# Kernel optimization log

Measured on AMD Instinct MI355X. Metric: run time of the kernel, lower is better.

## Reference

```python
import jax, jax.numpy as jnp
import numpy as np

N = 100000      # nodes
E = 1600000     # edges
NODE_DIM = 128
HID = 128
L = 3           # num_layers
B = 512         # graphs in batch
EPS = 1e-5      # LayerNorm eps


def setup_inputs() -> dict:
    key = jax.random.key(0)
    ks = jax.random.split(key, 8)
    nodes = jax.random.normal(ks[0], (N, NODE_DIM), jnp.float32)
    edges = jax.random.randint(ks[1], (2, E), 0, N, dtype=jnp.int32)
    edge_types = jax.random.randint(ks[2], (E,), 0, 10, dtype=jnp.int32)
    batch_idx = jnp.sort(jax.random.randint(ks[3], (N,), 0, B, dtype=jnp.int32))
    w_in = jax.random.normal(ks[4], (NODE_DIM, HID), jnp.float32) / np.sqrt(NODE_DIM)
    b_in = jnp.zeros((HID,), jnp.float32)
    gcn_w = jax.random.normal(ks[5], (L, HID, HID), jnp.float32) / np.sqrt(HID)
    gcn_b = jnp.zeros((L, HID), jnp.float32)
    ln_g = jnp.ones((L, HID), jnp.float32)
    ln_b = jnp.zeros((L, HID), jnp.float32)
    return {"nodes": nodes, "edges": edges, "edge_types": edge_types,
            "batch_idx": batch_idx, "w_in": w_in, "b_in": b_in,
            "gcn_w": gcn_w, "gcn_b": gcn_b, "ln_g": ln_g, "ln_b": ln_b}


def _layer_norm(x, g, b):
    mu = jnp.mean(x, axis=-1, keepdims=True)
    var = jnp.mean(jnp.square(x - mu), axis=-1, keepdims=True)
    return (x - mu) * jax.lax.rsqrt(var + EPS) * g + b


def reference(nodes, edges, edge_types, batch_idx, w_in, b_in, gcn_w, gcn_b, ln_g, ln_b):
    src, dst = edges[0], edges[1]
    # GCN normalization with self-loops: deg = in-degree(A) + 1
    deg = jax.ops.segment_sum(jnp.ones((E,), nodes.dtype), dst, num_segments=N) + 1.0
    dinv_sqrt = jax.lax.rsqrt(deg)
    dinv = 1.0 / deg                       # self-loop norm = 1/deg_i
    enorm = dinv_sqrt[src] * dinv_sqrt[dst]

    x = nodes @ w_in + b_in                # input projection [N, HID]
    for i in range(L):
        res = x
        xw = x @ gcn_w[i]
        agg = jax.ops.segment_sum(xw[src] * enorm[:, None], dst, num_segments=N)
        x = agg + xw * dinv[:, None] + gcn_b[i]
        x = jax.nn.relu(_layer_norm(x, ln_g[i], ln_b[i]))
        # dropout is identity in eval mode
        if i > 0:
            x = x + res                    # residual only for i > 0

    # global mean pool per graph
    counts = jax.ops.segment_sum(jnp.ones((N,), x.dtype), batch_idx, num_segments=B)
    plan = jax.ops.segment_sum(x, batch_idx, num_segments=B) / jnp.maximum(counts, 1.0)[:, None]
    return x, plan
```

## Files before the change

### kernel.cpp

```cpp
#include <hip/hip_runtime.h>
#include <hip/hip_bf16.h>

typedef __attribute__((ext_vector_type(8))) short bf16x8;
typedef __attribute__((ext_vector_type(4))) float f32x4;
typedef __attribute__((ext_vector_type(2))) float f32x2;

#define K1_TILE 6144
#define NBCAP 4608

__device__ __forceinline__ unsigned short f2bf(float f) {
    union { unsigned int i; float f; } x; x.f = f;
    unsigned int r = (x.i + 0x7fffu + ((x.i >> 16) & 1u)) >> 16;
    return (unsigned short)r;
}
__device__ __forceinline__ float blo(unsigned int u) { return __uint_as_float(u << 16); }
__device__ __forceinline__ float bhi(unsigned int u) { return __uint_as_float(u & 0xffff0000u); }


__global__ __launch_bounds__(256) void bin_k(const int* __restrict__ src,
                                             const int* __restrict__ dst,
                                             int* __restrict__ bucket_cursor,
                                             int* __restrict__ bins,
                                             int E, int NB) {
    __shared__ int hist[512];
    __shared__ int gdiff[512];
    __shared__ int wsum[4];
    __shared__ int stage[K1_TILE];
    int tid = threadIdx.x;
    int base = blockIdx.x * K1_TILE;
    int cnt = min(K1_TILE, E - base);

    hist[tid] = 0; hist[tid + 256] = 0;
    __syncthreads();
    for (int i = tid; i < cnt; i += 256) atomicAdd(&hist[dst[base + i] >> 8], 1);
    __syncthreads();

    int h0 = hist[2 * tid], h1 = hist[2 * tid + 1];
    int v = h0 + h1;
    int lane = tid & 63, wid = tid >> 6;
    int s = v;
#pragma unroll
    for (int o = 1; o < 64; o <<= 1) { int n = __shfl_up(s, o); if (lane >= o) s += n; }
    if (lane == 63) wsum[wid] = s;
    __syncthreads();
    if (tid == 0) { int r = 0; for (int w = 0; w < 4; ++w) { int t2 = wsum[w]; wsum[w] = r; r += t2; } }
    __syncthreads();
    int lb0 = s + wsum[wid] - v;
    int lb1 = lb0 + h0;
    int b0 = 2 * tid, b1 = 2 * tid + 1;
    int gb0 = 0, gb1 = 0;
    if (h0 > 0 && b0 < NB) gb0 = atomicAdd(&bucket_cursor[b0], h0);
    if (h1 > 0 && b1 < NB) gb1 = atomicAdd(&bucket_cursor[b1], h1);
    __syncthreads();
    hist[b0] = lb0; hist[b1] = lb1;
    gdiff[b0] = gb0 - lb0; gdiff[b1] = gb1 - lb1;
    __syncthreads();

    for (int i = tid; i < cnt; i += 256) {
        int sv = src[base + i], dv = dst[base + i];
        int pos = atomicAdd(&hist[dv >> 8], 1);
        stage[pos] = ((dv & 255) << 24) | sv;
    }
    __syncthreads();

    for (int i = tid; i < cnt; i += 256) {
        int e = stage[i];
        int b = dst[base + i] >> 8;
        (void)b;
        break;
    }
    for (int b = tid; b < 512; b += 256) {
    }
    __syncthreads();
}


__global__ __launch_bounds__(256) void bin2_k(const int* __restrict__ src,
                                              const int* __restrict__ dst,
                                              int* __restrict__ bucket_cursor,
                                              int* __restrict__ bins,
                                              int E, int NB) {
    __shared__ int hist[512];
    __shared__ int lbase[513];
    __shared__ int gdiff[512];
    __shared__ int wsum[4];
    __shared__ int stage[K1_TILE];
    int tid = threadIdx.x;
    int base = blockIdx.x * K1_TILE;
    int cnt = min(K1_TILE, E - base);

    hist[tid] = 0; hist[tid + 256] = 0;
    __syncthreads();
    for (int i = tid; i < cnt; i += 256) atomicAdd(&hist[dst[base + i] >> 8], 1);
    __syncthreads();

    int h0 = hist[2 * tid], h1 = hist[2 * tid + 1];
    int v = h0 + h1;
    int lane = tid & 63, wid = tid >> 6;
    int s = v;
#pragma unroll
    for (int o = 1; o < 64; o <<= 1) { int n = __shfl_up(s, o); if (lane >= o) s += n; }
    if (lane == 63) wsum[wid] = s;
    __syncthreads();
    if (tid == 0) { int r = 0; for (int w = 0; w < 4; ++w) { int t2 = wsum[w]; wsum[w] = r; r += t2; } }
    __syncthreads();
    int lb0 = s + wsum[wid] - v;
    int lb1 = lb0 + h0;
    int b0 = 2 * tid, b1 = 2 * tid + 1;
    int gb0 = 0, gb1 = 0;
    if (h0 > 0 && b0 < NB) gb0 = atomicAdd(&bucket_cursor[b0], h0);
    if (h1 > 0 && b1 < NB) gb1 = atomicAdd(&bucket_cursor[b1], h1);
    __syncthreads();
    hist[b0] = lb0; hist[b1] = lb1;
    lbase[b0] = lb0; lbase[b1] = lb1;
    gdiff[b0] = gb0 - lb0; gdiff[b1] = gb1 - lb1;
    if (tid == 0) lbase[512] = cnt;
    __syncthreads();

    for (int i = tid; i < cnt; i += 256) {
        int sv = src[base + i], dv = dst[base + i];
        int pos = atomicAdd(&hist[dv >> 8], 1);
        stage[pos] = ((dv & 255) << 24) | sv;
    }
    __syncthreads();

    for (int i = tid; i < cnt; i += 256) {
        int lo = 0, hi = 512;
        while (lo + 1 < hi) { int mid = (lo + hi) >> 1; if (lbase[mid] <= i) lo = mid; else hi = mid; }
        int p = gdiff[lo] + i;
        if (p < NBCAP) bins[(size_t)lo * NBCAP + p] = stage[i];
    }
}


__global__ __launch_bounds__(256) void bucket_scan_k(const int* __restrict__ bucket_cursor,
                                                     int* __restrict__ bucket_base, int NB) {
    __shared__ int wsum[4];
    int tid = threadIdx.x;
    int h0 = (2 * tid < NB) ? min(bucket_cursor[2 * tid], NBCAP) : 0;
    int h1 = (2 * tid + 1 < NB) ? min(bucket_cursor[2 * tid + 1], NBCAP) : 0;
    int v = h0 + h1;
    int lane = tid & 63, wid = tid >> 6;
    int s = v;
#pragma unroll
    for (int o = 1; o < 64; o <<= 1) { int n = __shfl_up(s, o); if (lane >= o) s += n; }
    if (lane == 63) wsum[wid] = s;
    __syncthreads();
    if (tid == 0) { int r = 0; for (int w = 0; w < 4; ++w) { int t2 = wsum[w]; wsum[w] = r; r += t2; } }
    __syncthreads();
    int excl = s + wsum[wid] - v;
    if (2 * tid < NB) bucket_base[2 * tid] = excl;
    if (2 * tid + 1 < NB) bucket_base[2 * tid + 1] = excl + h0;
}


__global__ __launch_bounds__(256) void csr_build_k(const int* __restrict__ bins,
                                                   const int* __restrict__ bucket_cursor,
                                                   const int* __restrict__ bucket_base,
                                                   int* __restrict__ csr_src,
                                                   int* __restrict__ row_start,
                                                   float* __restrict__ dinv_sqrt,
                                                   float* __restrict__ dinv,
                                                   int N) {
    __shared__ int counts[256];
    __shared__ int cursor[256];
    __shared__ int wsum[4];
    __shared__ int lcsr[NBCAP];
    int b = blockIdx.x, tid = threadIdx.x;
    int cnt = min(bucket_cursor[b], NBCAP);
    int cbase = bucket_base[b];
    const int* my = bins + (size_t)b * NBCAP;

    counts[tid] = 0;
    __syncthreads();
    for (int i = tid; i < cnt; i += 256) atomicAdd(&counts[((unsigned)my[i]) >> 24], 1);
    __syncthreads();

    int v = counts[tid];
    int lane = tid & 63, wid = tid >> 6;
    int s = v;
#pragma unroll
    for (int o = 1; o < 64; o <<= 1) { int n = __shfl_up(s, o); if (lane >= o) s += n; }
    if (lane == 63) wsum[wid] = s;
    __syncthreads();
    if (tid == 0) { int r = 0; for (int w = 0; w < 4; ++w) { int t2 = wsum[w]; wsum[w] = r; r += t2; } }
    __syncthreads();
    int excl = s + wsum[wid] - v;

    int node = b * 256 + tid;
    if (node <= N) row_start[node] = cbase + excl;
    if (node < N) {
        float dg = (float)v + 1.0f;
        dinv_sqrt[node] = rsqrtf(dg);
        dinv[node] = 1.0f / dg;
    }
    cursor[tid] = excl;
    __syncthreads();

    for (int i = tid; i < cnt; i += 256) {
        int e = my[i];
        int pos = atomicAdd(&cursor[((unsigned)e) >> 24], 1);
        lcsr[pos] = e & 0xffffff;
    }
    __syncthreads();
    for (int i = tid; i < cnt; i += 256) csr_src[cbase + i] = lcsr[i];
}


__global__ __launch_bounds__(256) void pack_w_k(const float* __restrict__ w_in,
                                                const float* __restrict__ gcn_w,
                                                unsigned short* __restrict__ Wp) {
    int t = blockIdx.x * 256 + threadIdx.x;
    if (t >= 8192) return;
    int mat = t >> 11;
    int kb = (t >> 9) & 3;
    int ct = (t >> 6) & 7;
    int lane = t & 63;
    int q = lane >> 4, c = lane & 15;
    const float* W = (mat == 0) ? w_in : (gcn_w + (size_t)(mat - 1) * 16384);
    unsigned short o[8];
#pragma unroll
    for (int j = 0; j < 8; ++j)
        o[j] = f2bf(W[(size_t)(kb * 32 + q * 8 + j) * 128 + ct * 16 + c]);
    unsigned short* dstp = Wp + ((size_t)t) * 8;
#pragma unroll
    for (int j = 0; j < 8; ++j) dstp[j] = o[j];
}


__global__ __launch_bounds__(256) void proj_k(const float* __restrict__ A,
                                              const unsigned short* __restrict__ Wp,
                                              const float* __restrict__ bias,
                                              unsigned short* __restrict__ Cb,
                                              int M) {
    __shared__ unsigned short stage[64 * 128];
    int wid = threadIdx.x >> 6, lane = threadIdx.x & 63;
    int blk0 = blockIdx.x * 64;
    int r0 = blk0 + wid * 16;
    int q = lane >> 4, c = lane & 15;
    int ar = min(r0 + c, M - 1);

    f32x4 acc[8];
#pragma unroll
    for (int ct = 0; ct < 8; ++ct) acc[ct] = (f32x4){0.f, 0.f, 0.f, 0.f};

#pragma unroll
    for (int kb = 0; kb < 4; ++kb) {
        float4 f0 = *(const float4*)&A[(size_t)ar * 128 + kb * 32 + q * 8];
        float4 f1 = *(const float4*)&A[(size_t)ar * 128 + kb * 32 + q * 8 + 4];
        union { unsigned short u[8]; bf16x8 v; } af;
        af.u[0] = f2bf(f0.x); af.u[1] = f2bf(f0.y); af.u[2] = f2bf(f0.z); af.u[3] = f2bf(f0.w);
        af.u[4] = f2bf(f1.x); af.u[5] = f2bf(f1.y); af.u[6] = f2bf(f1.z); af.u[7] = f2bf(f1.w);
#pragma unroll
        for (int ct = 0; ct < 8; ++ct) {
            bf16x8 b = *(const bf16x8*)&Wp[(((size_t)(kb * 8 + ct)) * 64 + lane) * 8];
            acc[ct] = __builtin_amdgcn_mfma_f32_16x16x32_bf16(af.v, b, acc[ct], 0, 0, 0);
        }
    }

#pragma unroll
    for (int ct = 0; ct < 8; ++ct) {
        int col = ct * 16 + c;
        float bv = bias[col];
#pragma unroll
        for (int r = 0; r < 4; ++r)
            stage[(wid * 16 + q * 4 + r) * 128 + col] = f2bf(acc[ct][r] + bv);
    }
    __syncthreads();

    int tid = threadIdx.x;
#pragma unroll
    for (int i = 0; i < 4; ++i) {
        int k = tid + i * 256;
        int row = k >> 4, colc = (k & 15) * 8;
        int grow = blk0 + row;
        if (grow < M)
            *(uint4*)&Cb[(size_t)grow * 128 + colc] = *(const uint4*)&stage[row * 128 + colc];
    }
}


__global__ __launch_bounds__(256) void gemmln_k(const unsigned short* __restrict__ S,
                                                unsigned short* xb16,
                                                float* __restrict__ xout,
                                                const unsigned short* __restrict__ Wp,
                                                const float* __restrict__ bias,
                                                const float* __restrict__ g,
                                                const float* __restrict__ bb,
                                                int M, int residual, int write_f32) {
    __shared__ unsigned short stage[64 * 128];
    int wid = threadIdx.x >> 6, lane = threadIdx.x & 63;
    int blk0 = blockIdx.x * 64;
    int r0 = blk0 + wid * 16;
    int q = lane >> 4, c = lane & 15;
    int ar = min(r0 + c, M - 1);

    f32x4 acc[8];
#pragma unroll
    for (int ct = 0; ct < 8; ++ct) acc[ct] = (f32x4){0.f, 0.f, 0.f, 0.f};

#pragma unroll
    for (int kb = 0; kb < 4; ++kb) {
        bf16x8 a = *(const bf16x8*)&S[(size_t)ar * 128 + kb * 32 + q * 8];
#pragma unroll
        for (int ct = 0; ct < 8; ++ct) {
            bf16x8 b = *(const bf16x8*)&Wp[(((size_t)(kb * 8 + ct)) * 64 + lane) * 8];
            acc[ct] = __builtin_amdgcn_mfma_f32_16x16x32_bf16(a, b, acc[ct], 0, 0, 0);
        }
    }

    float v[8][4];
#pragma unroll
    for (int ct = 0; ct < 8; ++ct) {
        float bv = bias[ct * 16 + c];
#pragma unroll
        for (int r = 0; r < 4; ++r) v[ct][r] = acc[ct][r] + bv;
    }

    float mu[4], rs[4];
#pragma unroll
    for (int r = 0; r < 4; ++r) {
        float s = 0.f;
#pragma unroll
        for (int ct = 0; ct < 8; ++ct) s += v[ct][r];
        s += __shfl_xor(s, 1); s += __shfl_xor(s, 2);
        s += __shfl_xor(s, 4); s += __shfl_xor(s, 8);
        mu[r] = s * (1.0f / 128.0f);
    }
#pragma unroll
    for (int r = 0; r < 4; ++r) {
        float s = 0.f;
#pragma unroll
        for (int ct = 0; ct < 8; ++ct) { float d = v[ct][r] - mu[r]; s += d * d; }
        s += __shfl_xor(s, 1); s += __shfl_xor(s, 2);
        s += __shfl_xor(s, 4); s += __shfl_xor(s, 8);
        rs[r] = rsqrtf(s * (1.0f / 128.0f) + 1e-5f);
    }

#pragma unroll
    for (int ct = 0; ct < 8; ++ct) {
        int col = ct * 16 + c;
        float gamma = g[col], beta = bb[col];
#pragma unroll
        for (int r = 0; r < 4; ++r) {
            float y = fmaxf((v[ct][r] - mu[r]) * rs[r] * gamma + beta, 0.f);
            stage[(wid * 16 + q * 4 + r) * 128 + col] = f2bf(y);
        }
    }
    __syncthreads();

    int tid = threadIdx.x;
#pragma unroll
    for (int i = 0; i < 4; ++i) {
        int k = tid + i * 256;
        int row = k >> 4, colc = (k & 15) * 8;
        int grow = blk0 + row;
        if (grow >= M) continue;
        uint4 sv = *(const uint4*)&stage[row * 128 + colc];
        float y0 = blo(sv.x), y1 = bhi(sv.x), y2 = blo(sv.y), y3 = bhi(sv.y);
        float y4 = blo(sv.z), y5 = bhi(sv.z), y6 = blo(sv.w), y7 = bhi(sv.w);
        if (residual) {
            uint4 rv = *(const uint4*)&xb16[(size_t)grow * 128 + colc];
            y0 += blo(rv.x); y1 += bhi(rv.x); y2 += blo(rv.y); y3 += bhi(rv.y);
            y4 += blo(rv.z); y5 += bhi(rv.z); y6 += blo(rv.w); y7 += bhi(rv.w);
        }
        union { unsigned short u[8]; uint4 qv; } o;
        o.u[0] = f2bf(y0); o.u[1] = f2bf(y1); o.u[2] = f2bf(y2); o.u[3] = f2bf(y3);
        o.u[4] = f2bf(y4); o.u[5] = f2bf(y5); o.u[6] = f2bf(y6); o.u[7] = f2bf(y7);
        *(uint4*)&xb16[(size_t)grow * 128 + colc] = o.qv;
        if (write_f32) {
            *(float4*)&xout[(size_t)grow * 128 + colc] = make_float4(y0, y1, y2, y3);
            *(float4*)&xout[(size_t)grow * 128 + colc + 4] = make_float4(y4, y5, y6, y7);
        }
    }
}


__device__ __forceinline__ void acc8(f32x2& a0, f32x2& a1, f32x2& a2, f32x2& a3,
                                     uint4 u, float w) {
    f32x2 w2 = {w, w};
    f32x2 p0 = {blo(u.x), bhi(u.x)};
    f32x2 p1 = {blo(u.y), bhi(u.y)};
    f32x2 p2 = {blo(u.z), bhi(u.z)};
    f32x2 p3 = {blo(u.w), bhi(u.w)};
    a0 += p0 * w2; a1 += p1 * w2; a2 += p2 * w2; a3 += p3 * w2;
}

__global__ __launch_bounds__(256) void agg_k(const unsigned short* __restrict__ xb16,
                                             unsigned short* __restrict__ S,
                                             const int* __restrict__ row_start,
                                             const int* __restrict__ csr_src,
                                             const float* __restrict__ dst_tbl,
                                             const float* __restrict__ dinv,
                                             int N) {
    int wid = threadIdx.x >> 6, lane = threadIdx.x & 63;
    int n = blockIdx.x * 4 + wid;
    if (n >= N) return;
    int grp = lane >> 4;
    int sl = lane & 15;
    int c0 = sl * 8;

    f32x2 a0 = {0.f, 0.f}, a1 = {0.f, 0.f}, a2 = {0.f, 0.f}, a3 = {0.f, 0.f};
    int beg = row_start[n], end = row_start[n + 1];

    int j = beg;
    for (; j + 8 <= end; j += 8) {
        int sa = csr_src[j + grp];
        int sb = csr_src[j + grp + 4];
        float wa = dst_tbl[sa];
        float wb = dst_tbl[sb];
        uint4 ua = *(const uint4*)&xb16[(size_t)sa * 128 + c0];
        uint4 ub = *(const uint4*)&xb16[(size_t)sb * 128 + c0];
        acc8(a0, a1, a2, a3, ua, wa);
        acc8(a0, a1, a2, a3, ub, wb);
    }
    if (j < end) {
        int ja = j + grp, jb = j + grp + 4;
        int jca = min(ja, end - 1), jcb = min(jb, end - 1);
        int sa = csr_src[jca];
        int sb = csr_src[jcb];
        float wa = (ja < end) ? dst_tbl[sa] : 0.f;
        float wb = (jb < end) ? dst_tbl[sb] : 0.f;
        uint4 ua = *(const uint4*)&xb16[(size_t)sa * 128 + c0];
        uint4 ub = *(const uint4*)&xb16[(size_t)sb * 128 + c0];
        acc8(a0, a1, a2, a3, ua, wa);
        acc8(a0, a1, a2, a3, ub, wb);
    }

#pragma unroll
    for (int o = 16; o <= 32; o <<= 1) {
        a0.x += __shfl_xor(a0.x, o); a0.y += __shfl_xor(a0.y, o);
        a1.x += __shfl_xor(a1.x, o); a1.y += __shfl_xor(a1.y, o);
        a2.x += __shfl_xor(a2.x, o); a2.y += __shfl_xor(a2.y, o);
        a3.x += __shfl_xor(a3.x, o); a3.y += __shfl_xor(a3.y, o);
    }

    if (grp == 0) {
        float dsd = dst_tbl[n];
        float di = dinv[n];
        uint4 u = *(const uint4*)&xb16[(size_t)n * 128 + c0];
        float y0 = a0.x * dsd + blo(u.x) * di;
        float y1 = a0.y * dsd + bhi(u.x) * di;
        float y2 = a1.x * dsd + blo(u.y) * di;
        float y3 = a1.y * dsd + bhi(u.y) * di;
        float y4 = a2.x * dsd + blo(u.z) * di;
        float y5 = a2.y * dsd + bhi(u.z) * di;
        float y6 = a3.x * dsd + blo(u.w) * di;
        float y7 = a3.y * dsd + bhi(u.w) * di;
        union { unsigned short us[8]; uint4 qv; } o;
        o.us[0] = f2bf(y0); o.us[1] = f2bf(y1); o.us[2] = f2bf(y2); o.us[3] = f2bf(y3);
        o.us[4] = f2bf(y4); o.us[5] = f2bf(y5); o.us[6] = f2bf(y6); o.us[7] = f2bf(y7);
        *(uint4*)&S[(size_t)n * 128 + c0] = o.qv;
    }
}


__global__ __launch_bounds__(256) void bounds_k(const int* __restrict__ bidx,
                                                int* __restrict__ gstart, int N, int B) {
    int i = blockIdx.x * 256 + threadIdx.x;
    if (i > N) return;
    int cur = (i < N) ? bidx[i] : B;
    int prev = (i == 0) ? -1 : bidx[i - 1];
    for (int b = prev + 1; b <= cur; ++b) gstart[b] = i;
}

__global__ __launch_bounds__(256) void pool_k(const unsigned short* __restrict__ x,
                                              const int* __restrict__ gstart,
                                              float* __restrict__ plan) {
    __shared__ float red[8 * 128];
    int b = blockIdx.x, t = threadIdx.x;
    int cg = (t & 31) * 4;
    int h = t >> 5;
    int s = gstart[b], e = gstart[b + 1];
    float acc0 = 0.f, acc1 = 0.f, acc2 = 0.f, acc3 = 0.f;
    for (int i = s + h; i < e; i += 8) {
        uint2 u = *(const uint2*)&x[(size_t)i * 128 + cg];
        acc0 += blo(u.x); acc1 += bhi(u.x); acc2 += blo(u.y); acc3 += bhi(u.y);
    }
    red[h * 128 + cg] = acc0; red[h * 128 + cg + 1] = acc1;
    red[h * 128 + cg + 2] = acc2; red[h * 128 + cg + 3] = acc3;
    __syncthreads();
    if (h == 0) {
#pragma unroll
        for (int k = 1; k < 8; ++k) {
            acc0 += red[k * 128 + cg];     acc1 += red[k * 128 + cg + 1];
            acc2 += red[k * 128 + cg + 2]; acc3 += red[k * 128 + cg + 3];
        }
        float inv = 1.0f / (float)max(e - s, 1);
        *(float4*)&plan[(size_t)b * 128 + cg] = make_float4(acc0 * inv, acc1 * inv,
                                                            acc2 * inv, acc3 * inv);
    }
}


extern "C" void kernel_launch(void* const* d_in, const int* in_sizes, int n_in,
                              void* d_out, int out_size, void* d_ws, size_t ws_size,
                              hipStream_t stream) {
    const float* nodes     = (const float*)d_in[0];
    const int*   edges     = (const int*)d_in[1];
    const int*   batch_idx = (const int*)d_in[3];
    const float* w_in      = (const float*)d_in[4];
    const float* b_in      = (const float*)d_in[5];
    const float* gcn_w     = (const float*)d_in[6];
    const float* gcn_b     = (const float*)d_in[7];
    const float* ln_g      = (const float*)d_in[8];
    const float* ln_b      = (const float*)d_in[9];

    const int N = in_sizes[0] / 128;
    const int E = in_sizes[1] / 2;
    const int B = out_size / 128 - N;
    const int* src = edges;
    const int* dst = edges + E;
    const int NB = (N + 256) / 256;

    float* xbuf = (float*)d_out;
    float* plan = xbuf + (size_t)N * 128;

    unsigned short* xb16 = (unsigned short*)d_ws;
    unsigned short* Sb   = xb16 + (size_t)N * 128;
    unsigned short* Wp   = Sb + (size_t)N * 128;
    int* bins            = (int*)(Wp + 4 * 16384);
    int* bucket_cursor   = bins + (size_t)NB * NBCAP;
    int* bucket_base     = bucket_cursor + NB;
    int* csr_src         = bucket_base + NB;
    int* row_start       = csr_src + E;
    float* dinv_sqrt     = (float*)(row_start + N + 1);
    float* dinv          = dinv_sqrt + N;
    int* gstart          = (int*)(dinv + N);

    hipMemsetAsync(bucket_cursor, 0, sizeof(int) * NB, stream);

    bin2_k<<<(E + K1_TILE - 1) / K1_TILE, 256, 0, stream>>>(src, dst, bucket_cursor, bins, E, NB);
    bucket_scan_k<<<1, 256, 0, stream>>>(bucket_cursor, bucket_base, NB);
    csr_build_k<<<NB, 256, 0, stream>>>(bins, bucket_cursor, bucket_base,
                                        csr_src, row_start, dinv_sqrt, dinv, N);

    pack_w_k<<<32, 256, 0, stream>>>(w_in, gcn_w, Wp);

    proj_k<<<(N + 63) / 64, 256, 0, stream>>>(nodes, Wp, b_in, xb16, N);

    for (int l = 0; l < 3; ++l) {
        agg_k<<<(N + 3) / 4, 256, 0, stream>>>(xb16, Sb, row_start, csr_src,
                                               dinv_sqrt, dinv, N);
        gemmln_k<<<(N + 63) / 64, 256, 0, stream>>>(Sb, xb16, xbuf,
                                                    Wp + (size_t)(l + 1) * 16384,
                                                    gcn_b + (size_t)l * 128,
                                                    ln_g + (size_t)l * 128,
                                                    ln_b + (size_t)l * 128, N,
                                                    l > 0 ? 1 : 0, l == 2 ? 1 : 0);
    }

    bounds_k<<<(N + 1 + 255) / 256, 256, 0, stream>>>(batch_idx, gstart, N, B);
    pool_k<<<B, 256, 0, stream>>>(xb16, gstart, plan);
}
```

Before: 460.4 us.

## Fuse neighbor aggregation with GEMM+LayerNorm per layer using ping-pong buffers

Merges the separate aggregation kernel and the GEMM+LayerNorm kernel into one kernel. Each wave aggregates 16 destination rows into padded LDS, then runs the MFMA GEMM, LayerNorm, ReLU and residual on them. Two ping-pong bf16 buffers replace the in-place update, which removes the intermediate S round trip through global memory and one launch per layer. In exchange each block now does serial per-row gathers, which may cut latency hiding and occupancy. LayerNorm variance now uses a single pass (E[x^2]-mu^2), and the unused bin_k kernel is deleted.

```diff
diff --git a/kernel.cpp b/kernel.cpp
--- a/kernel.cpp
+++ b/kernel.cpp
@@ -7,6 +7,7 @@
 
 #define K1_TILE 6144
 #define NBCAP 4608
+#define RSTRIDE 136
 
 __device__ __forceinline__ unsigned short f2bf(float f) {
     union { unsigned int i; float f; } x; x.f = f;
@@ -15,64 +16,6 @@
 }
 __device__ __forceinline__ float blo(unsigned int u) { return __uint_as_float(u << 16); }
 __device__ __forceinline__ float bhi(unsigned int u) { return __uint_as_float(u & 0xffff0000u); }
-
-
-__global__ __launch_bounds__(256) void bin_k(const int* __restrict__ src,
-                                             const int* __restrict__ dst,
-                                             int* __restrict__ bucket_cursor,
-                                             int* __restrict__ bins,
-                                             int E, int NB) {
-    __shared__ int hist[512];
-    __shared__ int gdiff[512];
-    __shared__ int wsum[4];
-    __shared__ int stage[K1_TILE];
-    int tid = threadIdx.x;
-    int base = blockIdx.x * K1_TILE;
-    int cnt = min(K1_TILE, E - base);
-
-    hist[tid] = 0; hist[tid + 256] = 0;
-    __syncthreads();
-    for (int i = tid; i < cnt; i += 256) atomicAdd(&hist[dst[base + i] >> 8], 1);
-    __syncthreads();
-
-    int h0 = hist[2 * tid], h1 = hist[2 * tid + 1];
-    int v = h0 + h1;
-    int lane = tid & 63, wid = tid >> 6;
-    int s = v;
-#pragma unroll
-    for (int o = 1; o < 64; o <<= 1) { int n = __shfl_up(s, o); if (lane >= o) s += n; }
-    if (lane == 63) wsum[wid] = s;
-    __syncthreads();
-    if (tid == 0) { int r = 0; for (int w = 0; w < 4; ++w) { int t2 = wsum[w]; wsum[w] = r; r += t2; } }
-    __syncthreads();
-    int lb0 = s + wsum[wid] - v;
-    int lb1 = lb0 + h0;
-    int b0 = 2 * tid, b1 = 2 * tid + 1;
-    int gb0 = 0, gb1 = 0;
-    if (h0 > 0 && b0 < NB) gb0 = atomicAdd(&bucket_cursor[b0], h0);
-    if (h1 > 0 && b1 < NB) gb1 = atomicAdd(&bucket_cursor[b1], h1);
-    __syncthreads();
-    hist[b0] = lb0; hist[b1] = lb1;
-    gdiff[b0] = gb0 - lb0; gdiff[b1] = gb1 - lb1;
-    __syncthreads();
-
-    for (int i = tid; i < cnt; i += 256) {
-        int sv = src[base + i], dv = dst[base + i];
-        int pos = atomicAdd(&hist[dv >> 8], 1);
-        stage[pos] = ((dv & 255) << 24) | sv;
-    }
-    __syncthreads();
-
-    for (int i = tid; i < cnt; i += 256) {
-        int e = stage[i];
-        int b = dst[base + i] >> 8;
-        (void)b;
-        break;
-    }
-    for (int b = tid; b < 512; b += 256) {
-    }
-    __syncthreads();
-}
 
 
 __global__ __launch_bounds__(256) void bin2_k(const int* __restrict__ src,
@@ -280,102 +223,6 @@
 }
 
 
-__global__ __launch_bounds__(256) void gemmln_k(const unsigned short* __restrict__ S,
-                                                unsigned short* xb16,
-                                                float* __restrict__ xout,
-                                                const unsigned short* __restrict__ Wp,
-                                                const float* __restrict__ bias,
-                                                const float* __restrict__ g,
-                                                const float* __restrict__ bb,
-                                                int M, int residual, int write_f32) {
-    __shared__ unsigned short stage[64 * 128];
-    int wid = threadIdx.x >> 6, lane = threadIdx.x & 63;
-    int blk0 = blockIdx.x * 64;
-    int r0 = blk0 + wid * 16;
-    int q = lane >> 4, c = lane & 15;
-    int ar = min(r0 + c, M - 1);
-
-    f32x4 acc[8];
-#pragma unroll
-    for (int ct = 0; ct < 8; ++ct) acc[ct] = (f32x4){0.f, 0.f, 0.f, 0.f};
-
-#pragma unroll
-    for (int kb = 0; kb < 4; ++kb) {
-        bf16x8 a = *(const bf16x8*)&S[(size_t)ar * 128 + kb * 32 + q * 8];
-#pragma unroll
-        for (int ct = 0; ct < 8; ++ct) {
-            bf16x8 b = *(const bf16x8*)&Wp[(((size_t)(kb * 8 + ct)) * 64 + lane) * 8];
-            acc[ct] = __builtin_amdgcn_mfma_f32_16x16x32_bf16(a, b, acc[ct], 0, 0, 0);
-        }
-    }
-
-    float v[8][4];
-#pragma unroll
-    for (int ct = 0; ct < 8; ++ct) {
-        float bv = bias[ct * 16 + c];
-#pragma unroll
-        for (int r = 0; r < 4; ++r) v[ct][r] = acc[ct][r] + bv;
-    }
-
-    float mu[4], rs[4];
-#pragma unroll
-    for (int r = 0; r < 4; ++r) {
-        float s = 0.f;
-#pragma unroll
-        for (int ct = 0; ct < 8; ++ct) s += v[ct][r];
-        s += __shfl_xor(s, 1); s += __shfl_xor(s, 2);
-        s += __shfl_xor(s, 4); s += __shfl_xor(s, 8);
-        mu[r] = s * (1.0f / 128.0f);
-    }
-#pragma unroll
-    for (int r = 0; r < 4; ++r) {
-        float s = 0.f;
-#pragma unroll
-        for (int ct = 0; ct < 8; ++ct) { float d = v[ct][r] - mu[r]; s += d * d; }
-        s += __shfl_xor(s, 1); s += __shfl_xor(s, 2);
-        s += __shfl_xor(s, 4); s += __shfl_xor(s, 8);
-        rs[r] = rsqrtf(s * (1.0f / 128.0f) + 1e-5f);
-    }
-
-#pragma unroll
-    for (int ct = 0; ct < 8; ++ct) {
-        int col = ct * 16 + c;
-        float gamma = g[col], beta = bb[col];
-#pragma unroll
-        for (int r = 0; r < 4; ++r) {
-            float y = fmaxf((v[ct][r] - mu[r]) * rs[r] * gamma + beta, 0.f);
-            stage[(wid * 16 + q * 4 + r) * 128 + col] = f2bf(y);
-        }
-    }
-    __syncthreads();
-
-    int tid = threadIdx.x;
-#pragma unroll
-    for (int i = 0; i < 4; ++i) {
-        int k = tid + i * 256;
-        int row = k >> 4, colc = (k & 15) * 8;
-        int grow = blk0 + row;
-        if (grow >= M) continue;
-        uint4 sv = *(const uint4*)&stage[row * 128 + colc];
-        float y0 = blo(sv.x), y1 = bhi(sv.x), y2 = blo(sv.y), y3 = bhi(sv.y);
-        float y4 = blo(sv.z), y5 = bhi(sv.z), y6 = blo(sv.w), y7 = bhi(sv.w);
-        if (residual) {
-            uint4 rv = *(const uint4*)&xb16[(size_t)grow * 128 + colc];
-            y0 += blo(rv.x); y1 += bhi(rv.x); y2 += blo(rv.y); y3 += bhi(rv.y);
-            y4 += blo(rv.z); y5 += bhi(rv.z); y6 += blo(rv.w); y7 += bhi(rv.w);
-        }
-        union { unsigned short u[8]; uint4 qv; } o;
-        o.u[0] = f2bf(y0); o.u[1] = f2bf(y1); o.u[2] = f2bf(y2); o.u[3] = f2bf(y3);
-        o.u[4] = f2bf(y4); o.u[5] = f2bf(y5); o.u[6] = f2bf(y6); o.u[7] = f2bf(y7);
-        *(uint4*)&xb16[(size_t)grow * 128 + colc] = o.qv;
-        if (write_f32) {
-            *(float4*)&xout[(size_t)grow * 128 + colc] = make_float4(y0, y1, y2, y3);
-            *(float4*)&xout[(size_t)grow * 128 + colc + 4] = make_float4(y4, y5, y6, y7);
-        }
-    }
-}
-
-
 __device__ __forceinline__ void acc8(f32x2& a0, f32x2& a1, f32x2& a2, f32x2& a3,
                                      uint4 u, float w) {
     f32x2 w2 = {w, w};
@@ -386,71 +233,150 @@
     a0 += p0 * w2; a1 += p1 * w2; a2 += p2 * w2; a3 += p3 * w2;
 }
 
-__global__ __launch_bounds__(256) void agg_k(const unsigned short* __restrict__ xb16,
-                                             unsigned short* __restrict__ S,
-                                             const int* __restrict__ row_start,
-                                             const int* __restrict__ csr_src,
-                                             const float* __restrict__ dst_tbl,
-                                             const float* __restrict__ dinv,
-                                             int N) {
+__global__ __launch_bounds__(256) void agg_gemmln_k(const unsigned short* __restrict__ xin,
+                                                    unsigned short* __restrict__ xoutb,
+                                                    float* __restrict__ xoutf,
+                                                    const unsigned short* __restrict__ Wp,
+                                                    const int* __restrict__ row_start,
+                                                    const int* __restrict__ csr_src,
+                                                    const float* __restrict__ dst_tbl,
+                                                    const float* __restrict__ dinv,
+                                                    const float* __restrict__ bias,
+                                                    const float* __restrict__ g,
+                                                    const float* __restrict__ bb,
+                                                    int M, int residual, int write_f32) {
+    __shared__ unsigned short stage[4 * 16 * RSTRIDE];
     int wid = threadIdx.x >> 6, lane = threadIdx.x & 63;
-    int n = blockIdx.x * 4 + wid;
-    if (n >= N) return;
+    int blk0 = blockIdx.x * 64;
     int grp = lane >> 4;
     int sl = lane & 15;
     int c0 = sl * 8;
-
-    f32x2 a0 = {0.f, 0.f}, a1 = {0.f, 0.f}, a2 = {0.f, 0.f}, a3 = {0.f, 0.f};
-    int beg = row_start[n], end = row_start[n + 1];
-
-    int j = beg;
-    for (; j + 8 <= end; j += 8) {
-        int sa = csr_src[j + grp];
-        int sb = csr_src[j + grp + 4];
-        float wa = dst_tbl[sa];
-        float wb = dst_tbl[sb];
-        uint4 ua = *(const uint4*)&xb16[(size_t)sa * 128 + c0];
-        uint4 ub = *(const uint4*)&xb16[(size_t)sb * 128 + c0];
-        acc8(a0, a1, a2, a3, ua, wa);
-        acc8(a0, a1, a2, a3, ub, wb);
-    }
-    if (j < end) {
-        int ja = j + grp, jb = j + grp + 4;
-        int jca = min(ja, end - 1), jcb = min(jb, end - 1);
-        int sa = csr_src[jca];
-        int sb = csr_src[jcb];
-        float wa = (ja < end) ? dst_tbl[sa] : 0.f;
-        float wb = (jb < end) ? dst_tbl[sb] : 0.f;
-        uint4 ua = *(const uint4*)&xb16[(size_t)sa * 128 + c0];
-        uint4 ub = *(const uint4*)&xb16[(size_t)sb * 128 + c0];
-        acc8(a0, a1, a2, a3, ua, wa);
-        acc8(a0, a1, a2, a3, ub, wb);
-    }
-
-#pragma unroll
-    for (int o = 16; o <= 32; o <<= 1) {
-        a0.x += __shfl_xor(a0.x, o); a0.y += __shfl_xor(a0.y, o);
-        a1.x += __shfl_xor(a1.x, o); a1.y += __shfl_xor(a1.y, o);
-        a2.x += __shfl_xor(a2.x, o); a2.y += __shfl_xor(a2.y, o);
-        a3.x += __shfl_xor(a3.x, o); a3.y += __shfl_xor(a3.y, o);
-    }
-
-    if (grp == 0) {
-        float dsd = dst_tbl[n];
-        float di = dinv[n];
-        uint4 u = *(const uint4*)&xb16[(size_t)n * 128 + c0];
-        float y0 = a0.x * dsd + blo(u.x) * di;
-        float y1 = a0.y * dsd + bhi(u.x) * di;
-        float y2 = a1.x * dsd + blo(u.y) * di;
-        float y3 = a1.y * dsd + bhi(u.y) * di;
-        float y4 = a2.x * dsd + blo(u.z) * di;
-        float y5 = a2.y * dsd + bhi(u.z) * di;
-        float y6 = a3.x * dsd + blo(u.w) * di;
-        float y7 = a3.y * dsd + bhi(u.w) * di;
-        union { unsigned short us[8]; uint4 qv; } o;
-        o.us[0] = f2bf(y0); o.us[1] = f2bf(y1); o.us[2] = f2bf(y2); o.us[3] = f2bf(y3);
-        o.us[4] = f2bf(y4); o.us[5] = f2bf(y5); o.us[6] = f2bf(y6); o.us[7] = f2bf(y7);
-        *(uint4*)&S[(size_t)n * 128 + c0] = o.qv;
+    unsigned short* ws = stage + wid * (16 * RSTRIDE);
+
+    for (int t = 0; t < 16; ++t) {
+        int n = blk0 + wid * 16 + t;
+        int nc = min(n, M - 1);
+        f32x2 a0 = {0.f, 0.f}, a1 = {0.f, 0.f}, a2 = {0.f, 0.f}, a3 = {0.f, 0.f};
+        int beg = row_start[nc], end = row_start[nc + 1];
+        int j = beg;
+        for (; j + 8 <= end; j += 8) {
+            int sa = csr_src[j + grp];
+            int sb = csr_src[j + grp + 4];
+            float wa = dst_tbl[sa];
+            float wb = dst_tbl[sb];
+            uint4 ua = *(const uint4*)&xin[(size_t)sa * 128 + c0];
+            uint4 ub = *(const uint4*)&xin[(size_t)sb * 128 + c0];
+            acc8(a0, a1, a2, a3, ua, wa);
+            acc8(a0, a1, a2, a3, ub, wb);
+        }
+        if (j < end) {
+            int ja = j + grp, jb = j + grp + 4;
+            int jca = min(ja, end - 1), jcb = min(jb, end - 1);
+            int sa = csr_src[jca];
+            int sb = csr_src[jcb];
+            float wa = (ja < end) ? dst_tbl[sa] : 0.f;
+            float wb = (jb < end) ? dst_tbl[sb] : 0.f;
+            uint4 ua = *(const uint4*)&xin[(size_t)sa * 128 + c0];
+            uint4 ub = *(const uint4*)&xin[(size_t)sb * 128 + c0];
+            acc8(a0, a1, a2, a3, ua, wa);
+            acc8(a0, a1, a2, a3, ub, wb);
+        }
+#pragma unroll
+        for (int o = 16; o <= 32; o <<= 1) {
+            a0.x += __shfl_xor(a0.x, o); a0.y += __shfl_xor(a0.y, o);
+            a1.x += __shfl_xor(a1.x, o); a1.y += __shfl_xor(a1.y, o);
+            a2.x += __shfl_xor(a2.x, o); a2.y += __shfl_xor(a2.y, o);
+            a3.x += __shfl_xor(a3.x, o); a3.y += __shfl_xor(a3.y, o);
+        }
+        if (grp == 0) {
+            float dsd = dst_tbl[nc];
+            float di = dinv[nc];
+            uint4 u = *(const uint4*)&xin[(size_t)nc * 128 + c0];
+            union { unsigned short us[8]; uint4 qv; } o;
+            o.us[0] = f2bf(a0.x * dsd + blo(u.x) * di);
+            o.us[1] = f2bf(a0.y * dsd + bhi(u.x) * di);
+            o.us[2] = f2bf(a1.x * dsd + blo(u.y) * di);
+            o.us[3] = f2bf(a1.y * dsd + bhi(u.y) * di);
+            o.us[4] = f2bf(a2.x * dsd + blo(u.z) * di);
+            o.us[5] = f2bf(a2.y * dsd + bhi(u.z) * di);
+            o.us[6] = f2bf(a3.x * dsd + blo(u.w) * di);
+            o.us[7] = f2bf(a3.y * dsd + bhi(u.w) * di);
+            *(uint4*)&ws[t * RSTRIDE + c0] = o.qv;
+        }
+    }
+    __syncthreads();
+
+    int q = grp, c = sl;
+    f32x4 acc[8];
+#pragma unroll
+    for (int ct = 0; ct < 8; ++ct) acc[ct] = (f32x4){0.f, 0.f, 0.f, 0.f};
+
+#pragma unroll
+    for (int kb = 0; kb < 4; ++kb) {
+        bf16x8 a = *(const bf16x8*)&ws[c * RSTRIDE + kb * 32 + q * 8];
+#pragma unroll
+        for (int ct = 0; ct < 8; ++ct) {
+            bf16x8 b = *(const bf16x8*)&Wp[(((size_t)(kb * 8 + ct)) * 64 + lane) * 8];
+            acc[ct] = __builtin_amdgcn_mfma_f32_16x16x32_bf16(a, b, acc[ct], 0, 0, 0);
+        }
+    }
+
+    float v[8][4];
+#pragma unroll
+    for (int ct = 0; ct < 8; ++ct) {
+        float bv = bias[ct * 16 + c];
+#pragma unroll
+        for (int r = 0; r < 4; ++r) v[ct][r] = acc[ct][r] + bv;
+    }
+
+    float mu[4], rs[4];
+#pragma unroll
+    for (int r = 0; r < 4; ++r) {
+        float s = 0.f, ss = 0.f;
+#pragma unroll
+        for (int ct = 0; ct < 8; ++ct) { float x = v[ct][r]; s += x; ss += x * x; }
+        s += __shfl_xor(s, 1); ss += __shfl_xor(ss, 1);
+        s += __shfl_xor(s, 2); ss += __shfl_xor(ss, 2);
+        s += __shfl_xor(s, 4); ss += __shfl_xor(ss, 4);
+        s += __shfl_xor(s, 8); ss += __shfl_xor(ss, 8);
+        mu[r] = s * (1.0f / 128.0f);
+        float var = fmaxf(ss * (1.0f / 128.0f) - mu[r] * mu[r], 0.f);
+        rs[r] = rsqrtf(var + 1e-5f);
+    }
+
+#pragma unroll
+    for (int ct = 0; ct < 8; ++ct) {
+        int col = ct * 16 + c;
+        float gamma = g[col], beta = bb[col];
+#pragma unroll
+        for (int r = 0; r < 4; ++r) {
+            float y = fmaxf((v[ct][r] - mu[r]) * rs[r] * gamma + beta, 0.f);
+            ws[(q * 4 + r) * RSTRIDE + col] = f2bf(y);
+        }
+    }
+
+#pragma unroll
+    for (int i = 0; i < 4; ++i) {
+        int k = lane + i * 64;
+        int row = k >> 4, colc = (k & 15) * 8;
+        int grow = blk0 + wid * 16 + row;
+        if (grow >= M) continue;
+        uint4 sv = *(const uint4*)&ws[row * RSTRIDE + colc];
+        float y0 = blo(sv.x), y1 = bhi(sv.x), y2 = blo(sv.y), y3 = bhi(sv.y);
+        float y4 = blo(sv.z), y5 = bhi(sv.z), y6 = blo(sv.w), y7 = bhi(sv.w);
+        if (residual) {
+            uint4 rv = *(const uint4*)&xin[(size_t)grow * 128 + colc];
+            y0 += blo(rv.x); y1 += bhi(rv.x); y2 += blo(rv.y); y3 += bhi(rv.y);
+            y4 += blo(rv.z); y5 += bhi(rv.z); y6 += blo(rv.w); y7 += bhi(rv.w);
+        }
+        union { unsigned short u[8]; uint4 qv; } o;
+        o.u[0] = f2bf(y0); o.u[1] = f2bf(y1); o.u[2] = f2bf(y2); o.u[3] = f2bf(y3);
+        o.u[4] = f2bf(y4); o.u[5] = f2bf(y5); o.u[6] = f2bf(y6); o.u[7] = f2bf(y7);
+        *(uint4*)&xoutb[(size_t)grow * 128 + colc] = o.qv;
+        if (write_f32) {
+            *(float4*)&xoutf[(size_t)grow * 128 + colc] = make_float4(y0, y1, y2, y3);
+            *(float4*)&xoutf[(size_t)grow * 128 + colc + 4] = make_float4(y4, y5, y6, y7);
+        }
     }
 }
 
@@ -516,9 +442,9 @@
     float* xbuf = (float*)d_out;
     float* plan = xbuf + (size_t)N * 128;
 
-    unsigned short* xb16 = (unsigned short*)d_ws;
-    unsigned short* Sb   = xb16 + (size_t)N * 128;
-    unsigned short* Wp   = Sb + (size_t)N * 128;
+    unsigned short* xb_a = (unsigned short*)d_ws;
+    unsigned short* xb_b = xb_a + (size_t)N * 128;
+    unsigned short* Wp   = xb_b + (size_t)N * 128;
     int* bins            = (int*)(Wp + 4 * 16384);
     int* bucket_cursor   = bins + (size_t)NB * NBCAP;
     int* bucket_base     = bucket_cursor + NB;
@@ -537,19 +463,22 @@
 
     pack_w_k<<<32, 256, 0, stream>>>(w_in, gcn_w, Wp);
 
-    proj_k<<<(N + 63) / 64, 256, 0, stream>>>(nodes, Wp, b_in, xb16, N);
-
+    proj_k<<<(N + 63) / 64, 256, 0, stream>>>(nodes, Wp, b_in, xb_a, N);
+
+    unsigned short* xin = xb_a;
+    unsigned short* xout = xb_b;
     for (int l = 0; l < 3; ++l) {
-        agg_k<<<(N + 3) / 4, 256, 0, stream>>>(xb16, Sb, row_start, csr_src,
-                                               dinv_sqrt, dinv, N);
-        gemmln_k<<<(N + 63) / 64, 256, 0, stream>>>(Sb, xb16, xbuf,
-                                                    Wp + (size_t)(l + 1) * 16384,
-                                                    gcn_b + (size_t)l * 128,
-                                                    ln_g + (size_t)l * 128,
-                                                    ln_b + (size_t)l * 128, N,
-                                                    l > 0 ? 1 : 0, l == 2 ? 1 : 0);
+        agg_gemmln_k<<<(N + 63) / 64, 256, 0, stream>>>(xin, xout, xbuf,
+                                                        Wp + (size_t)(l + 1) * 16384,
+                                                        row_start, csr_src,
+                                                        dinv_sqrt, dinv,
+                                                        gcn_b + (size_t)l * 128,
+                                                        ln_g + (size_t)l * 128,
+                                                        ln_b + (size_t)l * 128, N,
+                                                        l > 0 ? 1 : 0, l == 2 ? 1 : 0);
+        unsigned short* t = xin; xin = xout; xout = t;
     }
 
     bounds_k<<<(N + 1 + 255) / 256, 256, 0, stream>>>(batch_idx, gstart, N, B);
-    pool_k<<<B, 256, 0, stream>>>(xb16, gstart, plan);
-}
+    pool_k<<<B, 256, 0, stream>>>(xin, gstart, plan);
+}
```

Result: slower. 642.2 us (+39.5%).
